# Performance work log

Hardware: AMD Instinct MI355X
Metric: run time of the kernel (lower is better)

## Reference

```python
import jax, jax.numpy as jnp
import numpy as np

N = 100000
E = 1600000
IN_CH = 128
HEADS = 4
OUT_CH = 32
NEG_SLOPE = 0.2


def setup_inputs() -> dict:
    key = jax.random.key(0)
    k1, k2, k3, k4 = jax.random.split(key, 4)
    x = jax.random.normal(k1, (N, IN_CH), dtype=jnp.float32)
    edge_index = jax.random.randint(k2, (2, E), 0, N, dtype=jnp.int64)
    # xavier-uniform-like init scales
    w_lim = float(np.sqrt(6.0 / (IN_CH + HEADS * OUT_CH)))
    a_lim = float(np.sqrt(6.0 / (HEADS + 2 * OUT_CH)))
    weight = jax.random.uniform(k3, (IN_CH, HEADS * OUT_CH), dtype=jnp.float32, minval=-w_lim, maxval=w_lim)
    att = jax.random.uniform(k4, (1, HEADS, 2 * OUT_CH), dtype=jnp.float32, minval=-a_lim, maxval=a_lim)
    bias = jnp.zeros((HEADS * OUT_CH,), dtype=jnp.float32)
    return {"x": x, "edge_index": edge_index, "weight": weight, "att": att, "bias": bias}


def reference(x, edge_index, weight, att, bias):
    n = x.shape[0]
    h = jnp.matmul(x, weight).reshape(n, HEADS, OUT_CH)  # [N, H, C]
    src, dst = edge_index[0], edge_index[1]
    x_src = h[src]  # [E, H, C]
    x_dst = h[dst]  # [E, H, C]
    # att is [1, H, 2C]; split so we never materialize the concat tensor
    att_src = att[:, :, :OUT_CH]  # [1, H, C]
    att_dst = att[:, :, OUT_CH:]  # [1, H, C]
    alpha = (x_src * att_src).sum(-1) + (x_dst * att_dst).sum(-1)  # [E, H]
    alpha = jnp.where(alpha >= 0, alpha, NEG_SLOPE * alpha)  # leaky_relu
    # segment softmax over edges grouped by dst
    seg_max = jax.ops.segment_max(alpha, dst, num_segments=n)  # [N, H]
    alpha = jnp.exp(alpha - seg_max[dst])
    seg_sum = jax.ops.segment_sum(alpha, dst, num_segments=n)  # [N, H]
    alpha = alpha / (seg_sum[dst] + 1e-16)
    # scatter-add weighted messages
    out = jax.ops.segment_sum(alpha[:, :, None] * x_src, dst, num_segments=n)  # [N, H, C]
    out = out.reshape(n, HEADS * OUT_CH)  # concat=True
    return out + bias
```

## Files before the change

kernel.cpp:

```cpp
#include <hip/hip_runtime.h>

#define N_NODES 100000
#define N_EDGES 1600000
#define IN_CH   128
#define HEADS   4
#define OUT_CH  32
#define HID     128
#define NEG_SLOPE 0.2f

#define BNODES  1024
#define NBUCK   ((N_NODES + BNODES - 1) / BNODES)
#define NBLK    256
#define EPB     (N_EDGES / NBLK)

typedef unsigned int  uint;
typedef unsigned short ushort;

__device__ __forceinline__ ushort f2bf(float f) {
    uint u = __float_as_uint(f);
    return (ushort)((u + 0x7FFFu + ((u >> 16) & 1u)) >> 16);
}

#define BM 64
#define BK 32
__global__ __launch_bounds__(256) void k_gemm(const float* __restrict__ x,
                                              const float* __restrict__ w,
                                              ushort* __restrict__ h) {
    __shared__ float xs[BK][BM + 4];
    __shared__ float wsld[BK][HID + 4];

    const int tid  = threadIdx.x;
    const int nodeBase = blockIdx.x * BM;
    const int c0 = (tid & 15) * 8;
    const int n0 = (tid >> 4) * 4;

    float acc[4][8];
#pragma unroll
    for (int i = 0; i < 4; i++)
#pragma unroll
        for (int j = 0; j < 8; j++) acc[i][j] = 0.0f;

    for (int k0 = 0; k0 < IN_CH; k0 += BK) {
#pragma unroll
        for (int l = 0; l < 2; l++) {
            int idx  = tid + l * 256;
            int row  = idx >> 3;
            int col4 = (idx & 7) * 4;
            int n = nodeBase + row;
            float4 v = make_float4(0.f, 0.f, 0.f, 0.f);
            if (n < N_NODES) v = *reinterpret_cast<const float4*>(x + (size_t)n * IN_CH + k0 + col4);
            xs[col4 + 0][row] = v.x;
            xs[col4 + 1][row] = v.y;
            xs[col4 + 2][row] = v.z;
            xs[col4 + 3][row] = v.w;
        }
#pragma unroll
        for (int l = 0; l < 4; l++) {
            int idx  = tid + l * 256;
            int row  = idx >> 5;
            int col4 = (idx & 31) * 4;
            float4 v = *reinterpret_cast<const float4*>(w + (size_t)(k0 + row) * HID + col4);
            *reinterpret_cast<float4*>(&wsld[row][col4]) = v;
        }
        __syncthreads();

#pragma unroll
        for (int kk = 0; kk < BK; kk++) {
            float4 xv = *reinterpret_cast<const float4*>(&xs[kk][n0]);
            float4 wa = *reinterpret_cast<const float4*>(&wsld[kk][c0]);
            float4 wb = *reinterpret_cast<const float4*>(&wsld[kk][c0 + 4]);
            float xr[4] = {xv.x, xv.y, xv.z, xv.w};
            float wr[8] = {wa.x, wa.y, wa.z, wa.w, wb.x, wb.y, wb.z, wb.w};
#pragma unroll
            for (int i = 0; i < 4; i++)
#pragma unroll
                for (int j = 0; j < 8; j++)
                    acc[i][j] = fmaf(xr[i], wr[j], acc[i][j]);
        }
        __syncthreads();
    }

#pragma unroll
    for (int i = 0; i < 4; i++) {
        int n = nodeBase + n0 + i;
        if (n < N_NODES) {
            uint4 pk;
            pk.x = (uint)f2bf(acc[i][0]) | ((uint)f2bf(acc[i][1]) << 16);
            pk.y = (uint)f2bf(acc[i][2]) | ((uint)f2bf(acc[i][3]) << 16);
            pk.z = (uint)f2bf(acc[i][4]) | ((uint)f2bf(acc[i][5]) << 16);
            pk.w = (uint)f2bf(acc[i][6]) | ((uint)f2bf(acc[i][7]) << 16);
            *reinterpret_cast<uint4*>(h + (size_t)n * HID + c0) = pk;
        }
    }
}

__global__ void k_scores(const ushort* __restrict__ h, const float* __restrict__ att,
                         float* __restrict__ s_src, float* __restrict__ s_dst) {
    int i = blockIdx.x * blockDim.x + threadIdx.x;
    if (i >= N_NODES * HEADS) return;
    int head = i & (HEADS - 1);
    const uint* hp = reinterpret_cast<const uint*>(h + (size_t)i * OUT_CH);
    const float* as = att + head * (2 * OUT_CH);
    const float* ad = as + OUT_CH;
    float ss = 0.f, sd = 0.f;
#pragma unroll
    for (int q = 0; q < 4; q++) {
        uint4 u = reinterpret_cast<const uint4*>(hp)[q];
        uint uv[4] = {u.x, u.y, u.z, u.w};
#pragma unroll
        for (int t = 0; t < 4; t++) {
            int c = q * 8 + t * 2;
            float f0 = __uint_as_float(uv[t] << 16);
            float f1 = __uint_as_float(uv[t] & 0xFFFF0000u);
            ss += f0 * as[c] + f1 * as[c + 1];
            sd += f0 * ad[c] + f1 * ad[c + 1];
        }
    }
    s_src[i] = ss;
    s_dst[i] = sd;
}

__global__ __launch_bounds__(256) void k_h0(const int* __restrict__ ei,
                                            int* __restrict__ hist) {
    __shared__ int cnt[NBUCK];
    int t = threadIdx.x;
    if (t < NBUCK) cnt[t] = 0;
    __syncthreads();
    int base = blockIdx.x * EPB;
    for (int e = base + t; e < base + EPB; e += 256)
        atomicAdd(&cnt[ei[N_EDGES + e] >> 10], 1);
    __syncthreads();
    if (t < NBUCK) hist[blockIdx.x * NBUCK + t] = cnt[t];
}

__global__ __launch_bounds__(128) void k_sc0(int* __restrict__ hist,
                                             int* __restrict__ bucket_base) {
    __shared__ int sm[128];
    int t = threadIdx.x;
    int total = 0;
    if (t < NBUCK) {
#pragma unroll 8
        for (int r = 0; r < NBLK; r++) total += hist[r * NBUCK + t];
    }
    sm[t] = total;
    __syncthreads();
    for (int off = 1; off < 128; off <<= 1) {
        int v = (t >= off) ? sm[t - off] : 0;
        __syncthreads();
        sm[t] += v;
        __syncthreads();
    }
    int excl = sm[t] - total;
    if (t < NBUCK) {
        bucket_base[t] = excl;
        int running = excl;
#pragma unroll 8
        for (int r = 0; r < NBLK; r++) {
            int tmp = hist[r * NBUCK + t];
            hist[r * NBUCK + t] = running;
            running += tmp;
        }
    }
    if (t == 0) bucket_base[NBUCK] = N_EDGES;
}

__global__ __launch_bounds__(256) void k_b1(const int* __restrict__ ei,
                                            const int* __restrict__ hist,
                                            int* __restrict__ packed) {
    __shared__ int cur[NBUCK];
    int t = threadIdx.x;
    if (t < NBUCK) cur[t] = hist[blockIdx.x * NBUCK + t];
    __syncthreads();
    int base = blockIdx.x * EPB;
    for (int e = base + t; e < base + EPB; e += 256) {
        int src = ei[e], dst = ei[N_EDGES + e];
        int pos = atomicAdd(&cur[dst >> 10], 1);
        packed[pos] = (src << 10) | (dst & (BNODES - 1));
    }
}

__global__ __launch_bounds__(256) void k_b2(const int* __restrict__ packed,
                                            const int* __restrict__ bucket_base,
                                            int* __restrict__ csr_src,
                                            int* __restrict__ row_start) {
    __shared__ int cnt[BNODES];
    __shared__ int cur[BNODES];
    __shared__ int sm[256];
    int b = blockIdx.x, t = threadIdx.x;
    int beg = bucket_base[b], end = bucket_base[b + 1];
#pragma unroll
    for (int j = 0; j < 4; j++) cnt[t * 4 + j] = 0;
    __syncthreads();
    for (int e = beg + t; e < end; e += 256)
        atomicAdd(&cnt[packed[e] & (BNODES - 1)], 1);
    __syncthreads();
    int c0 = cnt[t * 4], c1 = cnt[t * 4 + 1], c2 = cnt[t * 4 + 2], c3 = cnt[t * 4 + 3];
    int tot = c0 + c1 + c2 + c3;
    sm[t] = tot;
    __syncthreads();
    for (int off = 1; off < 256; off <<= 1) {
        int v = (t >= off) ? sm[t - off] : 0;
        __syncthreads();
        sm[t] += v;
        __syncthreads();
    }
    int p0 = beg + sm[t] - tot;
    int p1 = p0 + c0, p2 = p1 + c1, p3 = p2 + c2;
    cur[t * 4] = p0; cur[t * 4 + 1] = p1; cur[t * 4 + 2] = p2; cur[t * 4 + 3] = p3;
    int nodeb = b * BNODES + t * 4;
    int pv[4] = {p0, p1, p2, p3};
#pragma unroll
    for (int j = 0; j < 4; j++)
        if (nodeb + j <= N_NODES) row_start[nodeb + j] = pv[j];
    __syncthreads();
    for (int e = beg + t; e < end; e += 256) {
        int pk = packed[e];
        int pos = atomicAdd(&cur[pk & (BNODES - 1)], 1);
        csr_src[pos] = pk >> 10;
    }
}

__global__ __launch_bounds__(64) void k_agg(const int* __restrict__ row_start,
                                            const int* __restrict__ csr_src,
                                            const float* __restrict__ s_src,
                                            const float* __restrict__ s_dst,
                                            const ushort* __restrict__ h,
                                            const float* __restrict__ bias,
                                            float* __restrict__ out) {
    int n    = blockIdx.x;
    int lane = threadIdx.x;
    int head = lane >> 4;
    float sdh = s_dst[n * HEADS + head];
    int beg = row_start[n], end = row_start[n + 1];
    const uint* hrow = reinterpret_cast<const uint*>(h);

    float acc0 = 0.f, acc1 = 0.f, sum_w = 0.f;
#pragma unroll 4
    for (int j = beg; j < end; j++) {
        int src = csr_src[j];
        float ss = s_src[src * HEADS + head];
        float a  = ss + sdh;
        a = a >= 0.f ? a : NEG_SLOPE * a;
        float wgt = __expf(a);
        sum_w += wgt;
        uint u = hrow[(size_t)src * (HID / 2) + lane];
        acc0 = fmaf(wgt, __uint_as_float(u << 16), acc0);
        acc1 = fmaf(wgt, __uint_as_float(u & 0xFFFF0000u), acc1);
    }
    float inv = 1.0f / (sum_w + 1e-16f);
    int ch = lane * 2;
    float2 bv = *reinterpret_cast<const float2*>(bias + ch);
    float2 o;
    o.x = acc0 * inv + bv.x;
    o.y = acc1 * inv + bv.y;
    *reinterpret_cast<float2*>(out + (size_t)n * HID + ch) = o;
}

extern "C" void kernel_launch(void* const* d_in, const int* in_sizes, int n_in,
                              void* d_out, int out_size, void* d_ws, size_t ws_size,
                              hipStream_t stream) {
    const float* x    = (const float*)d_in[0];
    const int*   ei   = (const int*)  d_in[1];
    const float* w    = (const float*)d_in[2];
    const float* att  = (const float*)d_in[3];
    const float* bias = (const float*)d_in[4];
    float* out = (float*)d_out;

    char* p = (char*)d_ws;
    float* s_src    = (float*)p;  p += (size_t)N_NODES * HEADS * 4;
    float* s_dst    = (float*)p;  p += (size_t)N_NODES * HEADS * 4;
    ushort* h       = (ushort*)p; p += (size_t)N_NODES * HID * 2;
    int* csr_src    = (int*)p;    p += (size_t)N_EDGES * 4;
    int* packed     = (int*)p;    p += (size_t)N_EDGES * 4;
    int* hist       = (int*)p;    p += (size_t)NBLK * NBUCK * 4;
    int* row_start  = (int*)p;    p += (size_t)(N_NODES + 1) * 4;
    int* bucket_base= (int*)p;    p += (size_t)(NBUCK + 1) * 4;

    k_gemm<<<(N_NODES + BM - 1) / BM, 256, 0, stream>>>(x, w, h);
    k_scores<<<(N_NODES * HEADS + 255) / 256, 256, 0, stream>>>(h, att, s_src, s_dst);
    k_h0<<<NBLK, 256, 0, stream>>>(ei, hist);
    k_sc0<<<1, 128, 0, stream>>>(hist, bucket_base);
    k_b1<<<NBLK, 256, 0, stream>>>(ei, hist, packed);
    k_b2<<<NBUCK, 256, 0, stream>>>(packed, bucket_base, csr_src, row_start);
    k_agg<<<N_NODES, 64, 0, stream>>>(row_start, csr_src, s_src, s_dst, h, bias, out);
}
```

Baseline: 322.9 us.

## Fuse attention scores into GEMM epilogue and parallelize bucket prefix scan

Attention score dot products are now computed in the GEMM epilogue from the fp32 accumulators. Partial sums are reduced through shared-memory atomics, which removes the separate k_scores kernel and its re-read of h. The histogram is stored transposed, and the single-block serial scan over 256 rows per bucket is replaced by a per-bucket parallel scan plus a small totals scan. The bucket base is then added in k_b1. This adds an extra kernel launch, and the scores change slightly because they use fp32 values instead of bf16-rounded ones.

```diff
diff --git a/kernel.cpp b/kernel.cpp
--- a/kernel.cpp
+++ b/kernel.cpp
@@ -25,14 +25,24 @@
 #define BK 32
 __global__ __launch_bounds__(256) void k_gemm(const float* __restrict__ x,
                                               const float* __restrict__ w,
-                                              ushort* __restrict__ h) {
+                                              const float* __restrict__ att,
+                                              ushort* __restrict__ h,
+                                              float* __restrict__ s_src,
+                                              float* __restrict__ s_dst) {
     __shared__ float xs[BK][BM + 4];
     __shared__ float wsld[BK][HID + 4];
+    __shared__ float sred[BM][8];
 
     const int tid  = threadIdx.x;
     const int nodeBase = blockIdx.x * BM;
     const int c0 = (tid & 15) * 8;
     const int n0 = (tid >> 4) * 4;
+
+#pragma unroll
+    for (int l = 0; l < 2; l++) {
+        int idx = tid + l * 256;
+        sred[idx >> 3][idx & 7] = 0.0f;
+    }
 
     float acc[4][8];
 #pragma unroll
@@ -92,36 +102,44 @@
             *reinterpret_cast<uint4*>(h + (size_t)n * HID + c0) = pk;
         }
     }
-}
-
-__global__ void k_scores(const ushort* __restrict__ h, const float* __restrict__ att,
-                         float* __restrict__ s_src, float* __restrict__ s_dst) {
-    int i = blockIdx.x * blockDim.x + threadIdx.x;
-    if (i >= N_NODES * HEADS) return;
-    int head = i & (HEADS - 1);
-    const uint* hp = reinterpret_cast<const uint*>(h + (size_t)i * OUT_CH);
-    const float* as = att + head * (2 * OUT_CH);
-    const float* ad = as + OUT_CH;
-    float ss = 0.f, sd = 0.f;
-#pragma unroll
-    for (int q = 0; q < 4; q++) {
-        uint4 u = reinterpret_cast<const uint4*>(hp)[q];
-        uint uv[4] = {u.x, u.y, u.z, u.w};
-#pragma unroll
-        for (int t = 0; t < 4; t++) {
-            int c = q * 8 + t * 2;
-            float f0 = __uint_as_float(uv[t] << 16);
-            float f1 = __uint_as_float(uv[t] & 0xFFFF0000u);
-            ss += f0 * as[c] + f1 * as[c + 1];
-            sd += f0 * ad[c] + f1 * ad[c + 1];
-        }
-    }
-    s_src[i] = ss;
-    s_dst[i] = sd;
+
+    {
+        int head = c0 >> 5;
+        int cc0  = c0 & 31;
+        const float* as = att + head * (2 * OUT_CH) + cc0;
+        const float* ad = as + OUT_CH;
+        float av[8], dv[8];
+#pragma unroll
+        for (int j = 0; j < 8; j++) { av[j] = as[j]; dv[j] = ad[j]; }
+#pragma unroll
+        for (int i = 0; i < 4; i++) {
+            float pss = 0.f, psd = 0.f;
+#pragma unroll
+            for (int j = 0; j < 8; j++) {
+                pss = fmaf(acc[i][j], av[j], pss);
+                psd = fmaf(acc[i][j], dv[j], psd);
+            }
+            atomicAdd(&sred[n0 + i][head * 2], pss);
+            atomicAdd(&sred[n0 + i][head * 2 + 1], psd);
+        }
+        __syncthreads();
+#pragma unroll
+        for (int l = 0; l < 2; l++) {
+            int idx = tid + l * 256;
+            int node = idx >> 3, slot = idx & 7;
+            int n = nodeBase + node;
+            if (n < N_NODES) {
+                float v = sred[node][slot];
+                int hd = slot >> 1;
+                if (slot & 1) s_dst[n * HEADS + hd] = v;
+                else          s_src[n * HEADS + hd] = v;
+            }
+        }
+    }
 }
 
 __global__ __launch_bounds__(256) void k_h0(const int* __restrict__ ei,
-                                            int* __restrict__ hist) {
+                                            int* __restrict__ hist_t) {
     __shared__ int cnt[NBUCK];
     int t = threadIdx.x;
     if (t < NBUCK) cnt[t] = 0;
@@ -130,46 +148,50 @@
     for (int e = base + t; e < base + EPB; e += 256)
         atomicAdd(&cnt[ei[N_EDGES + e] >> 10], 1);
     __syncthreads();
-    if (t < NBUCK) hist[blockIdx.x * NBUCK + t] = cnt[t];
-}
-
-__global__ __launch_bounds__(128) void k_sc0(int* __restrict__ hist,
-                                             int* __restrict__ bucket_base) {
+    if (t < NBUCK) hist_t[t * NBLK + blockIdx.x] = cnt[t];
+}
+
+__global__ __launch_bounds__(256) void k_sc0a(int* __restrict__ hist_t,
+                                              int* __restrict__ bucket_tot) {
+    __shared__ int sm[256];
+    int b = blockIdx.x, t = threadIdx.x;
+    int v = hist_t[b * NBLK + t];
+    sm[t] = v;
+    __syncthreads();
+    for (int off = 1; off < 256; off <<= 1) {
+        int u = (t >= off) ? sm[t - off] : 0;
+        __syncthreads();
+        sm[t] += u;
+        __syncthreads();
+    }
+    hist_t[b * NBLK + t] = sm[t] - v;
+    if (t == 255) bucket_tot[b] = sm[255];
+}
+
+__global__ __launch_bounds__(128) void k_sc0b(const int* __restrict__ bucket_tot,
+                                              int* __restrict__ bucket_base) {
     __shared__ int sm[128];
     int t = threadIdx.x;
-    int total = 0;
-    if (t < NBUCK) {
-#pragma unroll 8
-        for (int r = 0; r < NBLK; r++) total += hist[r * NBUCK + t];
-    }
-    sm[t] = total;
+    int v = (t < NBUCK) ? bucket_tot[t] : 0;
+    sm[t] = v;
     __syncthreads();
     for (int off = 1; off < 128; off <<= 1) {
-        int v = (t >= off) ? sm[t - off] : 0;
-        __syncthreads();
-        sm[t] += v;
-        __syncthreads();
-    }
-    int excl = sm[t] - total;
-    if (t < NBUCK) {
-        bucket_base[t] = excl;
-        int running = excl;
-#pragma unroll 8
-        for (int r = 0; r < NBLK; r++) {
-            int tmp = hist[r * NBUCK + t];
-            hist[r * NBUCK + t] = running;
-            running += tmp;
-        }
-    }
+        int u = (t >= off) ? sm[t - off] : 0;
+        __syncthreads();
+        sm[t] += u;
+        __syncthreads();
+    }
+    if (t < NBUCK) bucket_base[t] = sm[t] - v;
     if (t == 0) bucket_base[NBUCK] = N_EDGES;
 }
 
 __global__ __launch_bounds__(256) void k_b1(const int* __restrict__ ei,
-                                            const int* __restrict__ hist,
+                                            const int* __restrict__ hist_t,
+                                            const int* __restrict__ bucket_base,
                                             int* __restrict__ packed) {
     __shared__ int cur[NBUCK];
     int t = threadIdx.x;
-    if (t < NBUCK) cur[t] = hist[blockIdx.x * NBUCK + t];
+    if (t < NBUCK) cur[t] = bucket_base[t] + hist_t[t * NBLK + blockIdx.x];
     __syncthreads();
     int base = blockIdx.x * EPB;
     for (int e = base + t; e < base + EPB; e += 256) {
@@ -272,15 +294,16 @@
     ushort* h       = (ushort*)p; p += (size_t)N_NODES * HID * 2;
     int* csr_src    = (int*)p;    p += (size_t)N_EDGES * 4;
     int* packed     = (int*)p;    p += (size_t)N_EDGES * 4;
-    int* hist       = (int*)p;    p += (size_t)NBLK * NBUCK * 4;
+    int* hist_t     = (int*)p;    p += (size_t)NBUCK * NBLK * 4;
     int* row_start  = (int*)p;    p += (size_t)(N_NODES + 1) * 4;
+    int* bucket_tot = (int*)p;    p += (size_t)NBUCK * 4;
     int* bucket_base= (int*)p;    p += (size_t)(NBUCK + 1) * 4;
 
-    k_gemm<<<(N_NODES + BM - 1) / BM, 256, 0, stream>>>(x, w, h);
-    k_scores<<<(N_NODES * HEADS + 255) / 256, 256, 0, stream>>>(h, att, s_src, s_dst);
-    k_h0<<<NBLK, 256, 0, stream>>>(ei, hist);
-    k_sc0<<<1, 128, 0, stream>>>(hist, bucket_base);
-    k_b1<<<NBLK, 256, 0, stream>>>(ei, hist, packed);
+    k_gemm<<<(N_NODES + BM - 1) / BM, 256, 0, stream>>>(x, w, att, h, s_src, s_dst);
+    k_h0<<<NBLK, 256, 0, stream>>>(ei, hist_t);
+    k_sc0a<<<NBUCK, 256, 0, stream>>>(hist_t, bucket_tot);
+    k_sc0b<<<1, 128, 0, stream>>>(bucket_tot, bucket_base);
+    k_b1<<<NBLK, 256, 0, stream>>>(ei, hist_t, bucket_base, packed);
     k_b2<<<NBUCK, 256, 0, stream>>>(packed, bucket_base, csr_src, row_start);
     k_agg<<<N_NODES, 64, 0, stream>>>(row_start, csr_src, s_src, s_dst, h, bias, out);
 }
```

Result: no change. 328.2 us (+1.6%).
